# Kernel tuning notes

Hardware: AMD Instinct MI355X
Metric: run time of the kernel (lower is better)

## Reference

```python
import jax, jax.numpy as jnp
import numpy as np

B, N, C_S, C_COND, C_Z, H = 2, 512, 1024, 512, 128, 16
D = C_S // H  # head dim = 64
INF = 1.0e8
EPS = 1e-5


def _ln(x, scale=None, bias=None):
    m = x.mean(-1, keepdims=True)
    v = ((x - m) ** 2).mean(-1, keepdims=True)
    y = (x - m) * jax.lax.rsqrt(v + EPS)
    if scale is not None:
        y = y * scale + bias
    return y


def setup_inputs() -> dict:
    key = jax.random.key(0)
    ks = jax.random.split(key, 16)
    s = 0.02
    return {
        'x': jax.random.normal(ks[0], (B, N, C_S), jnp.float32),
        'cond': jax.random.normal(ks[1], (B, N, C_COND), jnp.float32),
        'z': jax.random.normal(ks[2], (B, N, N, C_Z), jnp.float32),
        'x_mask': jnp.ones((B, N), jnp.float32),
        # AdaLN(c_s, c_cond): scale/shift from cond
        'gamma_w': jax.random.normal(ks[3], (C_COND, C_S), jnp.float32) * s,
        'gamma_b': jnp.zeros((C_S,), jnp.float32),
        'beta_w': jax.random.normal(ks[4], (C_COND, C_S), jnp.float32) * s,
        # ln_z affine
        'z_scale': jnp.ones((C_Z,), jnp.float32),
        'z_bias': jnp.zeros((C_Z,), jnp.float32),
        # projections (all bias-free per module)
        'w_q': jax.random.normal(ks[5], (C_S, H * D), jnp.float32) * s,
        'w_kv': jax.random.normal(ks[6], (C_S, 2 * H * D), jnp.float32) * s,
        'w_b': jax.random.normal(ks[7], (C_Z, H), jnp.float32) * s,
        'w_og': jax.random.normal(ks[8], (C_S, C_S), jnp.float32) * s,
        'w_out': jax.random.normal(ks[9], (C_S, C_S), jnp.float32) * s,
        # cond_gate has bias, init -2.0
        'w_cg': jax.random.normal(ks[10], (C_COND, C_S), jnp.float32) * s,
        'b_cg': jnp.full((C_S,), -2.0, jnp.float32),
        # Transition (SwiGLU, n=2)
        'ffn_scale': jnp.ones((C_S,), jnp.float32),
        'ffn_bias': jnp.zeros((C_S,), jnp.float32),
        'w_a': jax.random.normal(ks[11], (C_S, 2 * C_S), jnp.float32) * s,
        'w_b2': jax.random.normal(ks[12], (C_S, 2 * C_S), jnp.float32) * s,
        'w_o': jax.random.normal(ks[13], (2 * C_S, C_S), jnp.float32) * s,
    }


def reference(x, cond, z, x_mask, gamma_w, gamma_b, beta_w, z_scale, z_bias,
              w_q, w_kv, w_b, w_og, w_out, w_cg, b_cg,
              ffn_scale, ffn_bias, w_a, w_b2, w_o):
    # AdaLN: LN(x, no affine) modulated by cond (sigmoid-gated scale + shift)
    cond_n = _ln(cond)
    _x = _ln(x) * jax.nn.sigmoid(cond_n @ gamma_w + gamma_b) + cond_n @ beta_w
    _z = _ln(z, z_scale, z_bias)

    q = (_x @ w_q).reshape(B, N, H, D)
    kv = _x @ w_kv
    k = kv[..., :H * D].reshape(B, N, H, D)
    v = kv[..., H * D:].reshape(B, N, H, D)

    # pair bias [B,N,N,H] -> [B,H,Nq,Nk], plus additive mask (query & key)
    b = _z @ w_b
    b = b + INF * (x_mask[:, None, :, None] - 1.0)  # key mask
    b = b + INF * (x_mask[:, :, None, None] - 1.0)  # query mask
    bias = jnp.transpose(b, (0, 3, 1, 2))  # [B,H,Nq,Nk]

    scale = 1.0 / jnp.sqrt(jnp.asarray(D, x.dtype))
    scores = jnp.einsum('bqhd,bkhd->bhqk', q, k) * scale + bias
    attn = jax.nn.softmax(scores, axis=-1)
    update = jnp.einsum('bhqk,bkhd->bqhd', attn, v).reshape(B, N, C_S)

    update = (update * jax.nn.sigmoid(_x @ w_og)) @ w_out
    update = update * jax.nn.sigmoid(cond @ w_cg + b_cg)
    x = x + update  # dropout is identity in eval

    # Transition (SwiGLU, n=2), masked residual
    xl = _ln(x, ffn_scale, ffn_bias)
    ffn = (jax.nn.silu(xl @ w_a) * (xl @ w_b2)) @ w_o
    x = x + ffn * x_mask[..., None]
    return x
```

## Files before the change

kernel.cpp:

```cpp
#include <hip/hip_runtime.h>
#include <stdint.h>

typedef unsigned short u16;
typedef unsigned int u32;
typedef __attribute__((ext_vector_type(4))) float f32x4;
typedef __attribute__((ext_vector_type(4))) unsigned int u32x4;
typedef __attribute__((ext_vector_type(4))) unsigned short u16x4;
typedef __attribute__((ext_vector_type(8))) __bf16 bf16x8;

union Frag { u32x4 u; bf16x8 b; };

__device__ __forceinline__ u16 f2bf(float x) {
  u32 u = __float_as_uint(x);
  u32 r = (u + 0x7fffu + ((u >> 16) & 1u)) >> 16;
  return (u16)r;
}
__device__ __forceinline__ float bf2f(u16 v) {
  u32 u = ((u32)v) << 16;
  return __uint_as_float(u);
}
__device__ __forceinline__ float sigmoidf_(float x) { return 1.0f / (1.0f + __expf(-x)); }

__device__ __forceinline__ void gload16(const void* g, void* lds) {
  __builtin_amdgcn_global_load_lds((const __attribute__((address_space(1))) unsigned int*)g,
                                   (__attribute__((address_space(3))) unsigned int*)lds, 16, 0, 0);
}

template<int EPI, int MI, int NI>
__device__ __forceinline__ void gemm_body(int bx, int by,
                                          u16* As0, u16* As1, u16* Bs0, u16* Bs1,
                                          const u16* __restrict__ A, const u16* __restrict__ Bt,
                                          const float* __restrict__ bias,
                                          const float* __restrict__ e0, const float* __restrict__ e1,
                                          void* __restrict__ Cp, int M, int N, int K) {
  constexpr int BM = 32 * MI;
  constexpr int BN = 32 * NI;
  const int t = threadIdx.x, wave = t >> 6, lane = t & 63;
  const int lrow = lane & 15, lgrp = lane >> 4;
  const int m0 = bx * BM, n0 = by * BN;
  const int wr = (wave >> 1) * (16 * MI), wc = (wave & 1) * (16 * NI);

  const int srow = wave * 8 + (lane >> 3);
  const int scol = (((lane & 7) ^ (lane >> 3)) << 3);
  const u16* Ab = A + (size_t)(m0 + srow) * K + scol;
  const u16* Bb = Bt + (size_t)(n0 + srow) * K + scol;

  f32x4 acc[MI][NI] = {};

  auto stage = [&](int k0, u16* Asd, u16* Bsd) {
#pragma unroll
    for (int i = 0; i < MI; ++i) gload16(Ab + (size_t)i * 32 * K + k0, Asd + wave * 512 + i * 2048);
#pragma unroll
    for (int i = 0; i < NI; ++i) gload16(Bb + (size_t)i * 32 * K + k0, Bsd + wave * 512 + i * 2048);
  };
  auto compute = [&](const u16* Asr, const u16* Bsr) {
#pragma unroll
    for (int ks = 0; ks < 2; ++ks) {
      Frag af[MI], bf4[NI];
#pragma unroll
      for (int mi = 0; mi < MI; ++mi) {
        int row = wr + mi * 16 + lrow;
        int slot = ((ks << 2) + lgrp) ^ (row & 7);
        af[mi].u = *(const u32x4*)((const char*)Asr + row * 128 + (slot << 4));
      }
#pragma unroll
      for (int ni = 0; ni < NI; ++ni) {
        int row = wc + ni * 16 + lrow;
        int slot = ((ks << 2) + lgrp) ^ (row & 7);
        bf4[ni].u = *(const u32x4*)((const char*)Bsr + row * 128 + (slot << 4));
      }
#pragma unroll
      for (int mi = 0; mi < MI; ++mi)
#pragma unroll
        for (int ni = 0; ni < NI; ++ni)
          acc[mi][ni] = __builtin_amdgcn_mfma_f32_16x16x32_bf16(af[mi].b, bf4[ni].b, acc[mi][ni], 0, 0, 0);
    }
  };

  stage(0, As0, Bs0);
  __syncthreads();
  for (int k0 = 0; k0 < K; k0 += 128) {
    stage(k0 + 64, As1, Bs1);
    compute(As0, Bs0);
    __syncthreads();
    if (k0 + 128 < K) stage(k0 + 128, As0, Bs0);
    compute(As1, Bs1);
    __syncthreads();
  }

  if constexpr (EPI == 4 || EPI == 5) {
    const int half = N >> 1;
#pragma unroll
    for (int mi = 0; mi < MI; ++mi) {
#pragma unroll
      for (int np = 0; np < 2; ++np) {
        int j = ((n0 + wc) >> 1) + np * 16 + lrow;
        float bj = 0.0f;
        if (EPI == 5) bj = bias[j];
#pragma unroll
        for (int rg = 0; rg < 4; ++rg) {
          int row = m0 + wr + mi * 16 + lgrp * 4 + rg;
          float a = acc[mi][2 * np][rg];
          float b = acc[mi][2 * np + 1][rg];
          float val;
          if constexpr (EPI == 4) {
            val = a * sigmoidf_(a) * b;
          } else {
            float mean = e1[2 * row], rinv = e1[2 * row + 1];
            float lnx = (e0[(size_t)row * half + j] - mean) * rinv;
            val = lnx * sigmoidf_(a + bj) + b;
          }
          ((u16*)Cp)[(size_t)row * half + j] = f2bf(val);
        }
      }
    }
  } else if constexpr (EPI == 6) {
    u16* vTp = (u16*)bias;
    const bool isv = (n0 >= 2048) && (n0 < 3072);
#pragma unroll
    for (int mi = 0; mi < MI; ++mi) {
#pragma unroll
      for (int ni = 0; ni < NI; ++ni) {
        int col = n0 + wc + ni * 16 + lrow;
        int rowb = m0 + wr + mi * 16 + lgrp * 4;
        if (isv) {
          int h = (col - 2048) >> 6, d = col & 63;
          int b = rowb >> 9, n = rowb & 511;
          u16x4 o;
#pragma unroll
          for (int rg = 0; rg < 4; ++rg) o[rg] = f2bf(acc[mi][ni][rg]);
          *(u16x4*)(vTp + ((size_t)((b * 16 + h) * 64 + d)) * 512 + n) = o;
        } else {
#pragma unroll
          for (int rg = 0; rg < 4; ++rg)
            ((u16*)Cp)[(size_t)(rowb + rg) * N + col] = f2bf(acc[mi][ni][rg]);
        }
      }
    }
  } else {
#pragma unroll
    for (int mi = 0; mi < MI; ++mi) {
#pragma unroll
      for (int ni = 0; ni < NI; ++ni) {
        int col = n0 + wc + ni * 16 + lrow;
        float bv = 0.0f;
        if (EPI == 0 && bias) bv = bias[col];
#pragma unroll
        for (int rg = 0; rg < 4; ++rg) {
          int row = m0 + wr + mi * 16 + lgrp * 4 + rg;
          size_t idx = (size_t)row * N + col;
          float v = acc[mi][ni][rg];
          if constexpr (EPI == 0)      ((float*)Cp)[idx] = v + bv;
          else if constexpr (EPI == 1) ((u16*)Cp)[idx] = f2bf(v);
          else if constexpr (EPI == 2) ((float*)Cp)[idx] = e0[idx] + v * sigmoidf_(e1[idx]);
          else                         ((float*)Cp)[idx] = e0[idx] + v * e1[row];
        }
      }
    }
  }
  (void)M;
}

template<int EPI, int MI, int NI>
__global__ __launch_bounds__(256) void gemm_t(const u16* __restrict__ A, const u16* __restrict__ Bt,
                                              const float* __restrict__ bias,
                                              const float* __restrict__ e0, const float* __restrict__ e1,
                                              void* __restrict__ Cp, int M, int N, int K) {
  __shared__ u16 As0[32 * MI * 64], As1[32 * MI * 64];
  __shared__ u16 Bs0[32 * NI * 64], Bs1[32 * NI * 64];
  gemm_body<EPI, MI, NI>(blockIdx.x, blockIdx.y, As0, As1, Bs0, Bs1, A, Bt, bias, e0, e1, Cp, M, N, K);
}

__global__ __launch_bounds__(256) void gemm_adaln_cg(
    const u16* __restrict__ cnb, const u16* __restrict__ gbT, const float* __restrict__ gamma_b,
    const float* __restrict__ x, const float* __restrict__ xstat, u16* __restrict__ xbf,
    const u16* __restrict__ cb, const u16* __restrict__ cgT, const float* __restrict__ b_cg,
    float* __restrict__ cglin) {
  __shared__ u16 As0[64 * 64], As1[64 * 64];
  __shared__ u16 Bs0[128 * 64], Bs1[128 * 64];
  int id = blockIdx.x;
  if (id < 256) {
    gemm_body<5, 2, 4>(id & 15, id >> 4, As0, As1, Bs0, Bs1, cnb, gbT, gamma_b, x, xstat, xbf, 1024, 2048, 512);
  } else {
    id -= 256;
    gemm_body<0, 1, 2>(id & 31, id >> 5, As0, As1, Bs0, Bs1, cb, cgT, b_cg, nullptr, nullptr, cglin, 1024, 1024, 512);
  }
}

__device__ __forceinline__ void wtrans_body(
    int id, float (*T)[65],
    const float* __restrict__ gamma_w, const float* __restrict__ beta_w,
    const float* __restrict__ w_cg, const float* __restrict__ w_q,
    const float* __restrict__ w_kv, const float* __restrict__ w_og,
    const float* __restrict__ w_out, const float* __restrict__ w_a,
    const float* __restrict__ w_b2, const float* __restrict__ w_o,
    u16* __restrict__ gbT, u16* __restrict__ cgT, u16* __restrict__ qkvT,
    u16* __restrict__ woT, u16* __restrict__ abT, u16* __restrict__ oT) {
  const float* src; u16* dst; int K, N, ptype = 0;
  if (id < 128)       { src = gamma_w; dst = gbT;  K = 512;  N = 1024; ptype = 1; }
  else if (id < 256)  { src = beta_w;  dst = gbT;  K = 512;  N = 1024; ptype = 2; id -= 128; }
  else if (id < 384)  { src = w_cg;    dst = cgT;  K = 512;  N = 1024; id -= 256; }
  else if (id < 640)  { src = w_q;     dst = qkvT; K = 1024; N = 1024; id -= 384; }
  else if (id < 1152) { src = w_kv;    dst = qkvT + (size_t)1024 * 1024; K = 1024; N = 2048; id -= 640; }
  else if (id < 1408) { src = w_og;    dst = qkvT + (size_t)3072 * 1024; K = 1024; N = 1024; id -= 1152; }
  else if (id < 1664) { src = w_out;   dst = woT;  K = 1024; N = 1024; id -= 1408; }
  else if (id < 2176) { src = w_a;     dst = abT;  K = 1024; N = 2048; ptype = 1; id -= 1664; }
  else if (id < 2688) { src = w_b2;    dst = abT;  K = 1024; N = 2048; ptype = 2; id -= 2176; }
  else                { src = w_o;     dst = oT;   K = 2048; N = 1024; id -= 2688; }
  const int tk = K >> 6;
  const int k0 = (id % tk) * 64, n0 = (id / tk) * 64;

  const int t = threadIdx.x;
#pragma unroll
  for (int i = 0; i < 4; ++i) {
    int idx = i * 256 + t;
    int kr = idx >> 4, c4 = (idx & 15) << 2;
    f32x4 v = *(const f32x4*)(src + (size_t)(k0 + kr) * N + n0 + c4);
    T[kr][c4] = v.x; T[kr][c4 + 1] = v.y; T[kr][c4 + 2] = v.z; T[kr][c4 + 3] = v.w;
  }
  __syncthreads();
#pragma unroll
  for (int i = 0; i < 2; ++i) {
    int idx = i * 256 + t;
    int n = idx >> 3, kc = (idx & 7) << 3;
    u32x4 o;
#pragma unroll
    for (int j = 0; j < 4; ++j) {
      u16 lo = f2bf(T[kc + 2 * j][n]);
      u16 hi = f2bf(T[kc + 2 * j + 1][n]);
      o[j] = (u32)lo | ((u32)hi << 16);
    }
    int ng = n0 + n;
    int r = (ptype == 0) ? ng : (((ng >> 4) << 5) + (ng & 15) + ((ptype == 2) ? 16 : 0));
    *(u32x4*)(dst + (size_t)r * K + k0 + kc) = o;
  }
}

__device__ __forceinline__ void block_reduce2_256(float& s, float& q, float* sb, int t) {
#pragma unroll
  for (int m = 1; m < 64; m <<= 1) { s += __shfl_xor(s, m); q += __shfl_xor(q, m); }
  if ((t & 63) == 0) { sb[(t >> 6) * 2] = s; sb[(t >> 6) * 2 + 1] = q; }
  __syncthreads();
  s = sb[0] + sb[2] + sb[4] + sb[6];
  q = sb[1] + sb[3] + sb[5] + sb[7];
}

__device__ __forceinline__ void ln_cond_x_body(int row, const float* __restrict__ cond,
                                               const float* __restrict__ x,
                                               u16* __restrict__ cnb, u16* __restrict__ cb,
                                               float* __restrict__ xstat) {
  const int t = threadIdx.x;
  __shared__ float sb[8];
  f32x4 xv = *(const f32x4*)(x + (size_t)row * 1024 + t * 4);
  float s = xv.x + xv.y + xv.z + xv.w;
  float q = xv.x * xv.x + xv.y * xv.y + xv.z * xv.z + xv.w * xv.w;
  block_reduce2_256(s, q, sb, t);
  if (t == 0) {
    float mean = s * (1.0f / 1024.0f);
    float var = q * (1.0f / 1024.0f) - mean * mean;
    xstat[2 * row] = mean;
    xstat[2 * row + 1] = rsqrtf(var + 1e-5f);
  }
  __syncthreads();
  f32x4 cv = {0.0f, 0.0f, 0.0f, 0.0f};
  if (t < 128) cv = *(const f32x4*)(cond + (size_t)row * 512 + t * 4);
  float s2 = cv.x + cv.y + cv.z + cv.w;
  float q2 = cv.x * cv.x + cv.y * cv.y + cv.z * cv.z + cv.w * cv.w;
  block_reduce2_256(s2, q2, sb, t);
  if (t < 128) {
    float mean = s2 * (1.0f / 512.0f);
    float var = q2 * (1.0f / 512.0f) - mean * mean;
    float rinv = rsqrtf(var + 1e-5f);
    u16x4 on, oc;
    on.x = f2bf((cv.x - mean) * rinv); on.y = f2bf((cv.y - mean) * rinv);
    on.z = f2bf((cv.z - mean) * rinv); on.w = f2bf((cv.w - mean) * rinv);
    oc.x = f2bf(cv.x); oc.y = f2bf(cv.y); oc.z = f2bf(cv.z); oc.w = f2bf(cv.w);
    *(u16x4*)(cnb + (size_t)row * 512 + t * 4) = on;
    *(u16x4*)(cb + (size_t)row * 512 + t * 4) = oc;
  }
}

__device__ __forceinline__ void biasz_body(int bq, const float* __restrict__ z,
                                           const float* __restrict__ zs, const float* __restrict__ zbias,
                                           const float* __restrict__ wb, const float* __restrict__ xmask,
                                           u16* __restrict__ biasb) {
  const int b = bq >> 9, qi = bq & 511;
  const int t = threadIdx.x, wave = t >> 6, lane = t & 63;
  const int lrow = lane & 15, lgrp = lane >> 4;

  float zsv[32], zbv[32];
  Frag wf[4];
#pragma unroll
  for (int j = 0; j < 4; ++j) {
#pragma unroll
    for (int e2 = 0; e2 < 4; ++e2) {
      int c0 = 32 * j + lgrp * 8 + e2 * 2;
      zsv[j * 8 + e2 * 2] = zs[c0];
      zsv[j * 8 + e2 * 2 + 1] = zs[c0 + 1];
      zbv[j * 8 + e2 * 2] = zbias[c0];
      zbv[j * 8 + e2 * 2 + 1] = zbias[c0 + 1];
      u16 lo = f2bf(wb[c0 * 16 + lrow]);
      u16 hi = f2bf(wb[(c0 + 1) * 16 + lrow]);
      wf[j].u[e2] = (u32)lo | ((u32)hi << 16);
    }
  }
  float qm = xmask[b * 512 + qi];
  float qadd = 1.0e8f * (qm - 1.0f);
  const float* zrowbase = z + ((size_t)(b * 512 + qi)) * 512 * 128;

  for (int kt = wave; kt < 32; kt += 4) {
    const float* zp = zrowbase + (size_t)(kt * 16 + lrow) * 128;
    float zv[32];
#pragma unroll
    for (int j = 0; j < 4; ++j) {
      f32x4 v0 = *(const f32x4*)(zp + 32 * j + lgrp * 8);
      f32x4 v1 = *(const f32x4*)(zp + 32 * j + lgrp * 8 + 4);
      zv[j * 8 + 0] = v0.x; zv[j * 8 + 1] = v0.y; zv[j * 8 + 2] = v0.z; zv[j * 8 + 3] = v0.w;
      zv[j * 8 + 4] = v1.x; zv[j * 8 + 5] = v1.y; zv[j * 8 + 6] = v1.z; zv[j * 8 + 7] = v1.w;
    }
    float s = 0.0f, q2 = 0.0f;
#pragma unroll
    for (int i = 0; i < 32; ++i) { s += zv[i]; q2 += zv[i] * zv[i]; }
    s += __shfl_xor(s, 16); q2 += __shfl_xor(q2, 16);
    s += __shfl_xor(s, 32); q2 += __shfl_xor(q2, 32);
    float mean = s * (1.0f / 128.0f);
    float var = q2 * (1.0f / 128.0f) - mean * mean;
    float rinv = rsqrtf(var + 1e-5f);

    f32x4 acc = {0.0f, 0.0f, 0.0f, 0.0f};
#pragma unroll
    for (int j = 0; j < 4; ++j) {
      Frag afr;
#pragma unroll
      for (int e2 = 0; e2 < 4; ++e2) {
        float zn0 = (zv[j * 8 + e2 * 2] - mean) * rinv * zsv[j * 8 + e2 * 2] + zbv[j * 8 + e2 * 2];
        float zn1 = (zv[j * 8 + e2 * 2 + 1] - mean) * rinv * zsv[j * 8 + e2 * 2 + 1] + zbv[j * 8 + e2 * 2 + 1];
        afr.u[e2] = (u32)f2bf(zn0) | ((u32)f2bf(zn1) << 16);
      }
      acc = __builtin_amdgcn_mfma_f32_16x16x32_bf16(afr.b, wf[j].b, acc, 0, 0, 0);
    }

    int kbase = kt * 16 + lgrp * 4;
    float v0 = acc[0] + qadd + 1.0e8f * (xmask[b * 512 + kbase + 0] - 1.0f);
    float v1 = acc[1] + qadd + 1.0e8f * (xmask[b * 512 + kbase + 1] - 1.0f);
    float v2 = acc[2] + qadd + 1.0e8f * (xmask[b * 512 + kbase + 2] - 1.0f);
    float v3 = acc[3] + qadd + 1.0e8f * (xmask[b * 512 + kbase + 3] - 1.0f);
    u16* outp = biasb + (((size_t)(b * 16 + lrow) * 512 + qi) * 512 + kbase);
    *(u32*)outp       = (u32)f2bf(v0) | ((u32)f2bf(v1) << 16);
    *(u32*)(outp + 2) = (u32)f2bf(v2) | ((u32)f2bf(v3) << 16);
  }
}

__global__ __launch_bounds__(256) void mega0(
    const float* __restrict__ z, const float* __restrict__ zs, const float* __restrict__ zbias,
    const float* __restrict__ wb, const float* __restrict__ xmask, u16* __restrict__ biasb,
    const float* __restrict__ gamma_w, const float* __restrict__ beta_w,
    const float* __restrict__ w_cg, const float* __restrict__ w_q,
    const float* __restrict__ w_kv, const float* __restrict__ w_og,
    const float* __restrict__ w_out, const float* __restrict__ w_a,
    const float* __restrict__ w_b2, const float* __restrict__ w_o,
    u16* __restrict__ gbT, u16* __restrict__ cgT, u16* __restrict__ qkvT,
    u16* __restrict__ woT, u16* __restrict__ abT, u16* __restrict__ oT,
    const float* __restrict__ cond, const float* __restrict__ x,
    u16* __restrict__ cnb, u16* __restrict__ cb, float* __restrict__ xstat) {
  __shared__ float Tsh[64][65];
  int id = blockIdx.x;
  if (id < 1024) {
    biasz_body(id, z, zs, zbias, wb, xmask, biasb);
  } else if (id < 4224) {
    wtrans_body(id - 1024, Tsh, gamma_w, beta_w, w_cg, w_q, w_kv, w_og, w_out, w_a, w_b2, w_o,
                gbT, cgT, qkvT, woT, abT, oT);
  } else {
    ln_cond_x_body(id - 4224, cond, x, cnb, cb, xstat);
  }
}

__global__ __launch_bounds__(256) void attn(const u16* __restrict__ qkv, const u16* __restrict__ vT,
                                            const u16* __restrict__ biasb, u16* __restrict__ gub) {
  __shared__ u16 Ks[64 * 64];
  __shared__ u16 Vs[64 * 64];
  __shared__ u16 Ps[4][16 * 64];
  __shared__ u16 Bbs[64 * 64];
  const int t = threadIdx.x, wave = t >> 6, lane = t & 63;
  const int lrow = lane & 15, lgrp = lane >> 4;
  const int bh = blockIdx.x >> 3, qt = blockIdx.x & 7;
  const int b = bh >> 4, h = bh & 15;
  const int q0 = qt * 64 + wave * 16;

  Frag qf[2];
#pragma unroll
  for (int ks = 0; ks < 2; ++ks) {
    int tok = b * 512 + q0 + lrow;
    qf[ks].u = *(const u32x4*)(qkv + (size_t)tok * 4096 + h * 64 + ks * 32 + lgrp * 8);
  }
  f32x4 oacc[4] = {};
  float mrun[4], lrun[4];
#pragma unroll
  for (int rg = 0; rg < 4; ++rg) { mrun[rg] = -3.0e38f; lrun[rg] = 0.0f; }

  const int o0 = t * 16, o1 = 4096 + t * 16;
  const int r0 = o0 >> 7, s0 = (o0 >> 4) & 7;
  const int r1 = o1 >> 7, s1 = (o1 >> 4) & 7;
  const int c0 = (s0 ^ (r0 & 7)) << 3;
  const int c1 = (s1 ^ (r1 & 7)) << 3;
  const int br0 = t >> 3, bs0 = t & 7;
  const int br1 = 32 + (t >> 3);
  const u16* bbase = biasb + ((size_t)bh * 512 + qt * 64) * 512;

  const u16* kp0 = qkv + (size_t)(b * 512 + r0) * 4096 + 1024 + h * 64 + c0;
  const u16* kp1 = qkv + (size_t)(b * 512 + r1) * 4096 + 1024 + h * 64 + c1;
  const u16* vp0 = vT + (size_t)(bh * 64 + r0) * 512 + c0;
  const u16* vp1 = vT + (size_t)(bh * 64 + r1) * 512 + c1;
  const u16* bp0 = bbase + (size_t)br0 * 512 + bs0 * 8;
  const u16* bp1 = bbase + (size_t)br1 * 512 + bs0 * 8;

  u32x4 kv0 = *(const u32x4*)(kp0);
  u32x4 kv1 = *(const u32x4*)(kp1);
  u32x4 vv0 = *(const u32x4*)(vp0);
  u32x4 vv1 = *(const u32x4*)(vp1);
  u32x4 bb0 = *(const u32x4*)(bp0);
  u32x4 bb1 = *(const u32x4*)(bp1);

  for (int kt = 0; kt < 8; ++kt) {
    __syncthreads();
    *(u32x4*)((char*)Ks + o0) = kv0;
    *(u32x4*)((char*)Ks + o1) = kv1;
    *(u32x4*)((char*)Vs + o0) = vv0;
    *(u32x4*)((char*)Vs + o1) = vv1;
    *(u32x4*)((char*)Bbs + br0 * 128 + ((bs0 ^ (br0 & 7)) << 4)) = bb0;
    *(u32x4*)((char*)Bbs + br1 * 128 + ((bs0 ^ (br1 & 7)) << 4)) = bb1;
    __syncthreads();

    {
      int k1g = ((kt + 1) & 7) * 64;
      kv0 = *(const u32x4*)(kp0 + (size_t)k1g * 4096);
      kv1 = *(const u32x4*)(kp1 + (size_t)k1g * 4096);
      vv0 = *(const u32x4*)(vp0 + k1g);
      vv1 = *(const u32x4*)(vp1 + k1g);
      bb0 = *(const u32x4*)(bp0 + k1g);
      bb1 = *(const u32x4*)(bp1 + k1g);
    }

    f32x4 sf[4] = {};
#pragma unroll
    for (int ks = 0; ks < 2; ++ks) {
#pragma unroll
      for (int ni = 0; ni < 4; ++ni) {
        int row = ni * 16 + lrow;
        int slot = (ks * 4 + lgrp) ^ (row & 7);
        Frag kf;
        kf.u = *(const u32x4*)((const char*)Ks + row * 128 + (slot << 4));
        sf[ni] = __builtin_amdgcn_mfma_f32_16x16x32_bf16(qf[ks].b, kf.b, sf[ni], 0, 0, 0);
      }
    }

    float sv[4][4];
#pragma unroll
    for (int ni = 0; ni < 4; ++ni) {
#pragma unroll
      for (int rg = 0; rg < 4; ++rg) {
        int qlocal = wave * 16 + lgrp * 4 + rg;
        int k = ni * 16 + lrow;
        float bvv = bf2f(*(const u16*)((const char*)Bbs + qlocal * 128 +
                                       (((k >> 3) ^ (qlocal & 7)) << 4) + (k & 7) * 2));
        sv[ni][rg] = sf[ni][rg] * 0.125f + bvv;
      }
    }
    float mnew[4], fac[4];
#pragma unroll
    for (int rg = 0; rg < 4; ++rg) {
      float tm = fmaxf(fmaxf(sv[0][rg], sv[1][rg]), fmaxf(sv[2][rg], sv[3][rg]));
      tm = fmaxf(tm, __shfl_xor(tm, 1));
      tm = fmaxf(tm, __shfl_xor(tm, 2));
      tm = fmaxf(tm, __shfl_xor(tm, 4));
      tm = fmaxf(tm, __shfl_xor(tm, 8));
      mnew[rg] = fmaxf(mrun[rg], tm);
      fac[rg] = __expf(mrun[rg] - mnew[rg]);
      mrun[rg] = mnew[rg];
    }
    float psum[4] = {0.0f, 0.0f, 0.0f, 0.0f};
#pragma unroll
    for (int ni = 0; ni < 4; ++ni)
#pragma unroll
      for (int rg = 0; rg < 4; ++rg) {
        float p = __expf(sv[ni][rg] - mnew[rg]);
        sv[ni][rg] = p;
        psum[rg] += p;
      }
#pragma unroll
    for (int rg = 0; rg < 4; ++rg) {
      float ps = psum[rg];
      ps += __shfl_xor(ps, 1); ps += __shfl_xor(ps, 2);
      ps += __shfl_xor(ps, 4); ps += __shfl_xor(ps, 8);
      lrun[rg] = lrun[rg] * fac[rg] + ps;
#pragma unroll
      for (int nd = 0; nd < 4; ++nd) oacc[nd][rg] *= fac[rg];
    }
#pragma unroll
    for (int ni = 0; ni < 4; ++ni)
#pragma unroll
      for (int rg = 0; rg < 4; ++rg) {
        int prow = lgrp * 4 + rg;
        int col = ni * 16 + lrow;
        int slot = (col >> 3) ^ (prow & 7);
        *(u16*)((char*)Ps[wave] + prow * 128 + (slot << 4) + (col & 7) * 2) = f2bf(sv[ni][rg]);
      }
    Frag paf[2];
#pragma unroll
    for (int ks = 0; ks < 2; ++ks) {
      int slot = (ks * 4 + lgrp) ^ (lrow & 7);
      paf[ks].u = *(const u32x4*)((const char*)Ps[wave] + lrow * 128 + (slot << 4));
    }
#pragma unroll
    for (int ks = 0; ks < 2; ++ks)
#pragma unroll
      for (int nd = 0; nd < 4; ++nd) {
        int row = nd * 16 + lrow;
        int slot = (ks * 4 + lgrp) ^ (row & 7);
        Frag vf;
        vf.u = *(const u32x4*)((const char*)Vs + row * 128 + (slot << 4));
        oacc[nd] = __builtin_amdgcn_mfma_f32_16x16x32_bf16(paf[ks].b, vf.b, oacc[nd], 0, 0, 0);
      }
  }

#pragma unroll
  for (int nd = 0; nd < 4; ++nd) {
#pragma unroll
    for (int rg = 0; rg < 4; ++rg) {
      int tok = b * 512 + q0 + lgrp * 4 + rg;
      int col = h * 64 + nd * 16 + lrow;
      float og = bf2f(qkv[(size_t)tok * 4096 + 3072 + col]);
      float val = oacc[nd][rg] / lrun[rg] * sigmoidf_(og);
      gub[(size_t)tok * 1024 + col] = f2bf(val);
    }
  }
}

__global__ __launch_bounds__(256) void ln_affine(const float* __restrict__ x1, const float* __restrict__ fs,
                                                 const float* __restrict__ fb, u16* __restrict__ xlb) {
  const int row = blockIdx.x;
  const int t = threadIdx.x;
  __shared__ float sb[8];
  f32x4 v = *(const f32x4*)(x1 + (size_t)row * 1024 + t * 4);
  float s = v.x + v.y + v.z + v.w;
  float q = v.x * v.x + v.y * v.y + v.z * v.z + v.w * v.w;
  block_reduce2_256(s, q, sb, t);
  float mean = s * (1.0f / 1024.0f);
  float var = q * (1.0f / 1024.0f) - mean * mean;
  float rinv = rsqrtf(var + 1e-5f);
  f32x4 fsv = *(const f32x4*)(fs + t * 4);
  f32x4 fbv = *(const f32x4*)(fb + t * 4);
  u16x4 o;
  o.x = f2bf((v.x - mean) * rinv * fsv.x + fbv.x);
  o.y = f2bf((v.y - mean) * rinv * fsv.y + fbv.y);
  o.z = f2bf((v.z - mean) * rinv * fsv.z + fbv.z);
  o.w = f2bf((v.w - mean) * rinv * fsv.w + fbv.w);
  *(u16x4*)(xlb + (size_t)row * 1024 + t * 4) = o;
}

extern "C" void kernel_launch(void* const* d_in, const int* in_sizes, int n_in,
                              void* d_out, int out_size, void* d_ws, size_t ws_size,
                              hipStream_t stream) {
  (void)in_sizes; (void)n_in; (void)out_size; (void)ws_size;
  const float* x        = (const float*)d_in[0];
  const float* cond     = (const float*)d_in[1];
  const float* z        = (const float*)d_in[2];
  const float* xmask    = (const float*)d_in[3];
  const float* gamma_w  = (const float*)d_in[4];
  const float* gamma_b  = (const float*)d_in[5];
  const float* beta_w   = (const float*)d_in[6];
  const float* z_scale  = (const float*)d_in[7];
  const float* z_bias   = (const float*)d_in[8];
  const float* w_q      = (const float*)d_in[9];
  const float* w_kv     = (const float*)d_in[10];
  const float* w_b      = (const float*)d_in[11];
  const float* w_og     = (const float*)d_in[12];
  const float* w_out    = (const float*)d_in[13];
  const float* w_cg     = (const float*)d_in[14];
  const float* b_cg     = (const float*)d_in[15];
  const float* ffn_scale= (const float*)d_in[16];
  const float* ffn_bias = (const float*)d_in[17];
  const float* w_a      = (const float*)d_in[18];
  const float* w_b2     = (const float*)d_in[19];
  const float* w_o      = (const float*)d_in[20];
  float* out = (float*)d_out;

  char* ws = (char*)d_ws;
  size_t off = 0;
  auto alloc = [&](size_t bytes) -> void* {
    void* p = ws + off;
    off += (bytes + 255) & ~(size_t)255;
    return p;
  };
  u16* cnb     = (u16*)alloc(1024 * 512 * 2);
  u16* cb      = (u16*)alloc(1024 * 512 * 2);
  float* xstat = (float*)alloc(1024 * 2 * 4);
  float* cglin = (float*)alloc((size_t)1024 * 1024 * 4);
  u16* xbf     = (u16*)alloc((size_t)1024 * 1024 * 2);
  u16* qkv     = (u16*)alloc((size_t)1024 * 4096 * 2);
  u16* vT      = (u16*)alloc((size_t)2048 * 512 * 2);
  u16* biasb   = (u16*)alloc((size_t)32 * 512 * 512 * 2);
  u16* gub     = (u16*)alloc((size_t)1024 * 1024 * 2);
  float* x1    = (float*)alloc((size_t)1024 * 1024 * 4);
  u16* xlb     = (u16*)alloc((size_t)1024 * 1024 * 2);
  u16* hb      = (u16*)alloc((size_t)1024 * 2048 * 2);
  u16* gbT     = (u16*)alloc((size_t)2048 * 512 * 2);
  u16* cgT     = (u16*)alloc((size_t)1024 * 512 * 2);
  u16* qkvT    = (u16*)alloc((size_t)4096 * 1024 * 2);
  u16* woT     = (u16*)alloc((size_t)1024 * 1024 * 2);
  u16* abT     = (u16*)alloc((size_t)4096 * 1024 * 2);
  u16* oT      = (u16*)alloc((size_t)1024 * 2048 * 2);

  mega0<<<5248, 256, 0, stream>>>(
      z, z_scale, z_bias, w_b, xmask, biasb,
      gamma_w, beta_w, w_cg, w_q, w_kv, w_og, w_out, w_a, w_b2, w_o,
      gbT, cgT, qkvT, woT, abT, oT,
      cond, x, cnb, cb, xstat);

  gemm_adaln_cg<<<768, 256, 0, stream>>>(cnb, gbT, gamma_b, x, xstat, xbf,
                                         cb, cgT, b_cg, cglin);

  gemm_t<6, 2, 4><<<dim3(16, 32), 256, 0, stream>>>(xbf, qkvT, (const float*)vT, nullptr, nullptr,
                                                    qkv, 1024, 4096, 1024);

  attn<<<256, 256, 0, stream>>>(qkv, vT, biasb, gub);

  gemm_t<2, 1, 2><<<dim3(32, 16), 256, 0, stream>>>(gub, woT, nullptr, x, cglin, x1, 1024, 1024, 1024);

  ln_affine<<<1024, 256, 0, stream>>>(x1, ffn_scale, ffn_bias, xlb);

  gemm_t<4, 2, 4><<<dim3(16, 32), 256, 0, stream>>>(xlb, abT, nullptr, nullptr, nullptr, hb, 1024, 4096, 1024);

  gemm_t<3, 1, 2><<<dim3(32, 16), 256, 0, stream>>>(hb, oT, nullptr, x1, xmask, out, 1024, 1024, 2048);
}
```

Before: 165.3 us.

## Split pair-bias computation across three launches to overlap with GEMMs

The z layernorm and pair-bias projection (biasz_body) previously ran as 1024 blocks inside the first mega kernel. It is now split into three chunks: 512 blocks stay in mega0, and 256 blocks each are folded into the AdaLN/cond-gate GEMM launch and the QKV GEMM launch. The aim is to overlap the memory-bound z read with the compute-bound GEMMs and fill idle CUs in the smaller GEMM grids. In exchange, the GEMM launches carry heterogeneous blocks that may interfere in cache and bandwidth or lengthen their tails.

```diff
diff --git a/kernel.cpp b/kernel.cpp
--- a/kernel.cpp
+++ b/kernel.cpp
@@ -169,22 +169,6 @@
   __shared__ u16 As0[32 * MI * 64], As1[32 * MI * 64];
   __shared__ u16 Bs0[32 * NI * 64], Bs1[32 * NI * 64];
   gemm_body<EPI, MI, NI>(blockIdx.x, blockIdx.y, As0, As1, Bs0, Bs1, A, Bt, bias, e0, e1, Cp, M, N, K);
-}
-
-__global__ __launch_bounds__(256) void gemm_adaln_cg(
-    const u16* __restrict__ cnb, const u16* __restrict__ gbT, const float* __restrict__ gamma_b,
-    const float* __restrict__ x, const float* __restrict__ xstat, u16* __restrict__ xbf,
-    const u16* __restrict__ cb, const u16* __restrict__ cgT, const float* __restrict__ b_cg,
-    float* __restrict__ cglin) {
-  __shared__ u16 As0[64 * 64], As1[64 * 64];
-  __shared__ u16 Bs0[128 * 64], Bs1[128 * 64];
-  int id = blockIdx.x;
-  if (id < 256) {
-    gemm_body<5, 2, 4>(id & 15, id >> 4, As0, As1, Bs0, Bs1, cnb, gbT, gamma_b, x, xstat, xbf, 1024, 2048, 512);
-  } else {
-    id -= 256;
-    gemm_body<0, 1, 2>(id & 31, id >> 5, As0, As1, Bs0, Bs1, cb, cgT, b_cg, nullptr, nullptr, cglin, 1024, 1024, 512);
-  }
 }
 
 __device__ __forceinline__ void wtrans_body(
@@ -365,13 +349,51 @@
     u16* __restrict__ cnb, u16* __restrict__ cb, float* __restrict__ xstat) {
   __shared__ float Tsh[64][65];
   int id = blockIdx.x;
-  if (id < 1024) {
+  if (id < 512) {
     biasz_body(id, z, zs, zbias, wb, xmask, biasb);
-  } else if (id < 4224) {
-    wtrans_body(id - 1024, Tsh, gamma_w, beta_w, w_cg, w_q, w_kv, w_og, w_out, w_a, w_b2, w_o,
+  } else if (id < 3712) {
+    wtrans_body(id - 512, Tsh, gamma_w, beta_w, w_cg, w_q, w_kv, w_og, w_out, w_a, w_b2, w_o,
                 gbT, cgT, qkvT, woT, abT, oT);
   } else {
-    ln_cond_x_body(id - 4224, cond, x, cnb, cb, xstat);
+    ln_cond_x_body(id - 3712, cond, x, cnb, cb, xstat);
+  }
+}
+
+__global__ __launch_bounds__(256) void adaln_cg_b(
+    const u16* __restrict__ cnb, const u16* __restrict__ gbT, const float* __restrict__ gamma_b,
+    const float* __restrict__ x, const float* __restrict__ xstat, u16* __restrict__ xbf,
+    const u16* __restrict__ cb, const u16* __restrict__ cgT, const float* __restrict__ b_cg,
+    float* __restrict__ cglin,
+    const float* __restrict__ z, const float* __restrict__ zs, const float* __restrict__ zbias,
+    const float* __restrict__ wb, const float* __restrict__ xmask, u16* __restrict__ biasb) {
+  __shared__ u16 As0[64 * 64], As1[64 * 64];
+  __shared__ u16 Bs0[128 * 64], Bs1[128 * 64];
+  int id = blockIdx.x;
+  if (id < 256) {
+    biasz_body(512 + id, z, zs, zbias, wb, xmask, biasb);
+  } else if (id < 512) {
+    id -= 256;
+    gemm_body<5, 2, 4>(id & 15, id >> 4, As0, As1, Bs0, Bs1, cnb, gbT, gamma_b, x, xstat, xbf, 1024, 2048, 512);
+  } else {
+    id -= 512;
+    gemm_body<0, 1, 2>(id & 31, id >> 5, As0, As1, Bs0, Bs1, cb, cgT, b_cg, nullptr, nullptr, cglin, 1024, 1024, 512);
+  }
+}
+
+__global__ __launch_bounds__(256) void qkv_b(
+    const u16* __restrict__ xbf, const u16* __restrict__ qkvT, u16* __restrict__ vT,
+    u16* __restrict__ qkv,
+    const float* __restrict__ z, const float* __restrict__ zs, const float* __restrict__ zbias,
+    const float* __restrict__ wb, const float* __restrict__ xmask, u16* __restrict__ biasb) {
+  __shared__ u16 As0[64 * 64], As1[64 * 64];
+  __shared__ u16 Bs0[128 * 64], Bs1[128 * 64];
+  int id = blockIdx.x;
+  if (id < 256) {
+    biasz_body(768 + id, z, zs, zbias, wb, xmask, biasb);
+  } else {
+    id -= 256;
+    gemm_body<6, 2, 4>(id & 15, id >> 4, As0, As1, Bs0, Bs1, xbf, qkvT, (const float*)vT,
+                       nullptr, nullptr, qkv, 1024, 4096, 1024);
   }
 }
 
@@ -611,17 +633,18 @@
   u16* abT     = (u16*)alloc((size_t)4096 * 1024 * 2);
   u16* oT      = (u16*)alloc((size_t)1024 * 2048 * 2);
 
-  mega0<<<5248, 256, 0, stream>>>(
+  mega0<<<4736, 256, 0, stream>>>(
       z, z_scale, z_bias, w_b, xmask, biasb,
       gamma_w, beta_w, w_cg, w_q, w_kv, w_og, w_out, w_a, w_b2, w_o,
       gbT, cgT, qkvT, woT, abT, oT,
       cond, x, cnb, cb, xstat);
 
-  gemm_adaln_cg<<<768, 256, 0, stream>>>(cnb, gbT, gamma_b, x, xstat, xbf,
-                                         cb, cgT, b_cg, cglin);
-
-  gemm_t<6, 2, 4><<<dim3(16, 32), 256, 0, stream>>>(xbf, qkvT, (const float*)vT, nullptr, nullptr,
-                                                    qkv, 1024, 4096, 1024);
+  adaln_cg_b<<<1024, 256, 0, stream>>>(cnb, gbT, gamma_b, x, xstat, xbf,
+                                       cb, cgT, b_cg, cglin,
+                                       z, z_scale, z_bias, w_b, xmask, biasb);
+
+  qkv_b<<<768, 256, 0, stream>>>(xbf, qkvT, vT, qkv,
+                                 z, z_scale, z_bias, w_b, xmask, biasb);
 
   attn<<<256, 256, 0, stream>>>(qkv, vT, biasb, gub);
 
```

Result: no change. 165.8 us (+0.3%).
